# Kernel tuning notes

Hardware: AMD Instinct MI355X
Metric: run time of the kernel (lower is better)

## Reference

```python
import jax, jax.numpy as jnp
import numpy as np

V = 50257
H = 1032          # hidden_size + 8
IN = 2 * H        # gru input size
S = 8192          # encoder seq len


def setup_inputs() -> dict:
    key = jax.random.key(0)
    ks = jax.random.split(key, 12)
    s = 0.02
    return {
        "word_input": jax.random.randint(ks[0], (1,), 0, V),
        "last_context": jax.random.normal(ks[1], (1, 1, H), jnp.float32),
        "prev_hidden": jax.random.normal(ks[2], (1, 1, H), jnp.float32),
        "encoder_outputs": jax.random.normal(ks[3], (S, 1, H), jnp.float32),
        "emb": jax.random.normal(ks[4], (V, H), jnp.float32) * s,
        "W_ih": jax.random.normal(ks[5], (3 * H, IN), jnp.float32) * s,
        "W_hh": jax.random.normal(ks[6], (3 * H, H), jnp.float32) * s,
        "b_ih": jnp.zeros((3 * H,), jnp.float32),
        "b_hh": jnp.zeros((3 * H,), jnp.float32),
        "W_a": jax.random.normal(ks[7], (H, H), jnp.float32) * s,
        "b_a": jnp.zeros((H,), jnp.float32),
        "W_out": jax.random.normal(ks[8], (V, 2 * H), jnp.float32) * s,
        "b_out": jnp.zeros((V,), jnp.float32),
    }


def reference(word_input, last_context, prev_hidden, encoder_outputs,
              emb, W_ih, W_hh, b_ih, b_hh, W_a, b_a, W_out, b_out):
    # --- embedding + concat with last context -> GRU input [1, 2H]
    embedded = emb[word_input].reshape(1, H)            # dropout = identity (eval)
    x = jnp.concatenate([embedded, last_context[0]], axis=1)   # [1, 2H]
    h = prev_hidden[0]                                  # [1, H]

    # --- single-step GRU (PyTorch gate layout: r, z, n)
    gx = x @ W_ih.T + b_ih                              # [1, 3H]
    gh = h @ W_hh.T + b_hh                              # [1, 3H]
    xr, xz, xn = jnp.split(gx, 3, axis=1)
    hr, hz, hn = jnp.split(gh, 3, axis=1)
    r = jax.nn.sigmoid(xr + hr)
    z = jax.nn.sigmoid(xz + hz)
    n = jnp.tanh(xn + r * hn)
    h_new = (1.0 - z) * n + z * h                       # [1, H]

    # --- Luong attention over all encoder steps in one batched matmul
    enc = encoder_outputs[:, 0, :]                      # [S, H]
    proj = enc @ W_a.T + b_a                            # [S, H]
    scores = proj @ h_new[0]                            # [S]
    attn_weights = jax.nn.softmax(scores)               # [S]
    attn_context = (attn_weights[:, None] * enc).sum(axis=0, keepdims=True)  # [1, H]

    # --- output projection + log softmax
    joined = jnp.concatenate([h_new, attn_context], axis=1)    # [1, 2H]
    output = jax.nn.log_softmax(joined @ W_out.T + b_out, axis=1)  # [1, V]

    current_hidden = h_new[None]                        # [1, 1, H]
    attn_w = attn_weights[None, None]                   # [1, 1, S]
    return output, attn_context[None], current_hidden, attn_w
```

## Files before the change

kernel.cpp:

```cpp
#include <hip/hip_runtime.h>
#include <math.h>

#define V  50257
#define H  1032
#define INW 2064
#define S  8192

#define O_CTX  50257
#define O_HID  51289
#define O_ATTN 52321

#define NPART 2048

__device__ __forceinline__ float waveReduceSum(float v) {
#pragma unroll
  for (int off = 32; off > 0; off >>= 1) v += __shfl_down(v, off);
  return v;
}

__global__ __launch_bounds__(256) void gru_kernel(
    const int* __restrict__ word, const float* __restrict__ emb,
    const float* __restrict__ lc, const float* __restrict__ ph,
    const float* __restrict__ W_ih, const float* __restrict__ W_hh,
    const float* __restrict__ b_ih, const float* __restrict__ b_hh,
    float* __restrict__ hnew, float* __restrict__ hid_out,
    float* __restrict__ v_acc) {
  int t = threadIdx.x, wave = t >> 6, lane = t & 63;
  if (blockIdx.x == 0) {
    for (int k = t; k < H; k += 256) v_acc[k] = 0.f;
  }
  int j = blockIdx.x * 4 + wave;

  const float4* erow = (const float4*)(emb + (size_t)word[0] * H);
  const float4* lc4  = (const float4*)lc;
  const float4* ph4  = (const float4*)ph;

  const float4* wr = (const float4*)(W_ih + (size_t)j * INW);
  const float4* wz = (const float4*)(W_ih + (size_t)(H + j) * INW);
  const float4* wn = (const float4*)(W_ih + (size_t)(2 * H + j) * INW);
  float sir = 0.f, siz = 0.f, sin_ = 0.f;
  for (int i = lane; i < INW / 4; i += 64) {
    float4 xv = (i < H / 4) ? erow[i] : lc4[i - H / 4];
    float4 a = wr[i]; sir  += xv.x * a.x + xv.y * a.y + xv.z * a.z + xv.w * a.w;
    float4 b = wz[i]; siz  += xv.x * b.x + xv.y * b.y + xv.z * b.z + xv.w * b.w;
    float4 c = wn[i]; sin_ += xv.x * c.x + xv.y * c.y + xv.z * c.z + xv.w * c.w;
  }
  const float4* ur = (const float4*)(W_hh + (size_t)j * H);
  const float4* uz = (const float4*)(W_hh + (size_t)(H + j) * H);
  const float4* un = (const float4*)(W_hh + (size_t)(2 * H + j) * H);
  float shr = 0.f, shz = 0.f, shn = 0.f;
  for (int i = lane; i < H / 4; i += 64) {
    float4 hv = ph4[i];
    float4 a = ur[i]; shr += hv.x * a.x + hv.y * a.y + hv.z * a.z + hv.w * a.w;
    float4 b = uz[i]; shz += hv.x * b.x + hv.y * b.y + hv.z * b.z + hv.w * b.w;
    float4 c = un[i]; shn += hv.x * c.x + hv.y * c.y + hv.z * c.z + hv.w * c.w;
  }
  sir = waveReduceSum(sir); siz = waveReduceSum(siz); sin_ = waveReduceSum(sin_);
  shr = waveReduceSum(shr); shz = waveReduceSum(shz); shn = waveReduceSum(shn);
  if (lane == 0) {
    float gr = (sir + b_ih[j])         + (shr + b_hh[j]);
    float gz = (siz + b_ih[H + j])     + (shz + b_hh[H + j]);
    float r  = 1.f / (1.f + expf(-gr));
    float z  = 1.f / (1.f + expf(-gz));
    float n  = tanhf((sin_ + b_ih[2 * H + j]) + r * (shn + b_hh[2 * H + j]));
    float hv = (1.f - z) * n + z * ph[j];
    hnew[j] = hv;
    hid_out[j] = hv;
  }
}

__global__ __launch_bounds__(256) void va_kernel(
    const float* __restrict__ W_a, const float* __restrict__ hnew,
    float* __restrict__ v, float* __restrict__ ctx) {
  int k = blockIdx.x * 256 + threadIdx.x;
  if (k >= H) return;
  if (blockIdx.y == 0) ctx[k] = 0.f;
  int j0 = blockIdx.y * 65;
  int j1 = min(j0 + 65, H);
  float acc = 0.f;
  for (int j = j0; j < j1; ++j) acc += W_a[(size_t)j * H + k] * hnew[j];
  atomicAdd(&v[k], acc);
}

__global__ __launch_bounds__(256) void scores_kernel(
    const float* __restrict__ enc, const float* __restrict__ v,
    float* __restrict__ scores) {
  int t = threadIdx.x, wave = t >> 6, lane = t & 63;
  int s = blockIdx.x * 4 + wave;
  const float4* row = (const float4*)(enc + (size_t)s * H);
  const float4* v4  = (const float4*)v;
  float acc = 0.f;
  for (int i = lane; i < H / 4; i += 64) {
    float4 a = row[i], b = v4[i];
    acc += a.x * b.x + a.y * b.y + a.z * b.z + a.w * b.w;
  }
  acc = waveReduceSum(acc);
  if (lane == 0) scores[s] = acc;
}

__global__ __launch_bounds__(256) void ctx_kernel(
    const float* __restrict__ enc, const float* __restrict__ scores,
    float* __restrict__ ctx, float* __restrict__ attn_out) {
  __shared__ float red[256];
  __shared__ float wsh[64];
  int t = threadIdx.x;
  float m = -3.4e38f;
  for (int i = t; i < S; i += 256) m = fmaxf(m, scores[i]);
  red[t] = m; __syncthreads();
  for (int off = 128; off; off >>= 1) {
    if (t < off) red[t] = fmaxf(red[t], red[t + off]);
    __syncthreads();
  }
  m = red[0]; __syncthreads();
  float s = 0.f;
  for (int i = t; i < S; i += 256) s += expf(scores[i] - m);
  red[t] = s; __syncthreads();
  for (int off = 128; off; off >>= 1) {
    if (t < off) red[t] += red[t + off];
    __syncthreads();
  }
  float inv = 1.f / red[0];
  int s0 = blockIdx.y * 64;
  if (t < 64) wsh[t] = expf(scores[s0 + t] - m) * inv;
  __syncthreads();
  if (blockIdx.x == 0 && t < 64) attn_out[s0 + t] = wsh[t];
  int k = blockIdx.x * 256 + t;
  if (k < H) {
    float acc = 0.f;
    for (int si = 0; si < 64; ++si) acc += wsh[si] * enc[(size_t)(s0 + si) * H + k];
    atomicAdd(&ctx[k], acc);
  }
}

__global__ __launch_bounds__(256) void logits_kernel(
    const float* __restrict__ hnew, const float* __restrict__ ctx,
    const float* __restrict__ W_out, const float* __restrict__ b_out,
    float* __restrict__ out, float* __restrict__ ctx_out,
    float* __restrict__ partials) {
  __shared__ __align__(16) float joined[INW];
  __shared__ float wm[4], wsv[4];
  int t = threadIdx.x;
  for (int k = t; k < H; k += 256) {
    joined[k] = hnew[k];
    joined[H + k] = ctx[k];
  }
  if (blockIdx.x == 0) {
    for (int k = t; k < H; k += 256) ctx_out[k] = ctx[k];
  }
  __syncthreads();
  int lane = t & 63, wv = t >> 6;
  int gw = blockIdx.x * 4 + wv;
  const float4* j4 = (const float4*)joined;
  float lm = -3.4e38f, ls = 0.f;
  for (int vi = gw; vi < V; vi += NPART * 4) {
    const float4* row = (const float4*)(W_out + (size_t)vi * INW);
    float acc = 0.f;
    for (int i = lane; i < INW / 4; i += 64) {
      float4 a = row[i];
      float4 b = j4[i];
      acc += a.x * b.x + a.y * b.y + a.z * b.z + a.w * b.w;
    }
    acc = waveReduceSum(acc);
    if (lane == 0) {
      float x = acc + b_out[vi];
      out[vi] = x;
      float nm = fmaxf(lm, x);
      ls = ls * expf(lm - nm) + expf(x - nm);
      lm = nm;
    }
  }
  if (lane == 0) { wm[wv] = lm; wsv[wv] = ls; }
  __syncthreads();
  if (t == 0) {
    float m = wm[0], sb = wsv[0];
    for (int i = 1; i < 4; ++i) {
      float nm = fmaxf(m, wm[i]);
      sb = sb * expf(m - nm) + wsv[i] * expf(wm[i] - nm);
      m = nm;
    }
    partials[2 * blockIdx.x]     = m;
    partials[2 * blockIdx.x + 1] = sb;
  }
}

__global__ __launch_bounds__(256) void apply_kernel(
    float* __restrict__ out, const float* __restrict__ partials) {
  __shared__ float mm[256], ssv[256];
  int t = threadIdx.x;
  float m = -3.4e38f, s = 0.f;
  for (int i = t; i < NPART; i += 256) {
    float bm = partials[2 * i], bs = partials[2 * i + 1];
    float nm = fmaxf(m, bm);
    s = s * expf(m - nm) + bs * expf(bm - nm);
    m = nm;
  }
  mm[t] = m; ssv[t] = s; __syncthreads();
  for (int off = 128; off; off >>= 1) {
    if (t < off) {
      float m2 = mm[t + off], s2 = ssv[t + off];
      float nm = fmaxf(mm[t], m2);
      ssv[t] = ssv[t] * expf(mm[t] - nm) + s2 * expf(m2 - nm);
      mm[t] = nm;
    }
    __syncthreads();
  }
  float L = mm[0] + logf(ssv[0]);
  int i = blockIdx.x * 256 + t;
  if (i < V) out[i] -= L;
}

extern "C" void kernel_launch(void* const* d_in, const int* in_sizes, int n_in,
                              void* d_out, int out_size, void* d_ws, size_t ws_size,
                              hipStream_t stream) {
  const int*   word  = (const int*)d_in[0];
  const float* lc    = (const float*)d_in[1];
  const float* ph    = (const float*)d_in[2];
  const float* enc   = (const float*)d_in[3];
  const float* emb   = (const float*)d_in[4];
  const float* W_ih  = (const float*)d_in[5];
  const float* W_hh  = (const float*)d_in[6];
  const float* b_ih  = (const float*)d_in[7];
  const float* b_hh  = (const float*)d_in[8];
  const float* W_a   = (const float*)d_in[9];
  const float* W_out = (const float*)d_in[11];
  const float* b_out = (const float*)d_in[12];
  float* out = (float*)d_out;
  float* ws  = (float*)d_ws;

  float* hnew     = ws;
  float* v        = ws + 1032;
  float* scores   = ws + 2064;
  float* ctx      = ws + 10256;
  float* partials = ws + 11288;

  gru_kernel<<<258, 256, 0, stream>>>(word, emb, lc, ph, W_ih, W_hh, b_ih, b_hh,
                                      hnew, out + O_HID, v);
  va_kernel<<<dim3(5, 16), 256, 0, stream>>>(W_a, hnew, v, ctx);
  scores_kernel<<<2048, 256, 0, stream>>>(enc, v, scores);
  ctx_kernel<<<dim3(5, 128), 256, 0, stream>>>(enc, scores, ctx, out + O_ATTN);
  logits_kernel<<<NPART, 256, 0, stream>>>(hnew, ctx, W_out, b_out, out,
                                           out + O_CTX, partials);
  apply_kernel<<<(V + 255) / 256, 256, 0, stream>>>(out, partials);
}
```

Before: 156.5 us.

## Split GRU matvec across more waves and fuse gate nonlinearity into W_a pass

The GRU step now has one wave per half-row of each of the 3H gate rows, writing partial dot products to workspace. That replaces 258 blocks where each wave handled three gate rows serially. The gate nonlinearity is recomputed inside the W_a projection kernel, which fuses the h_new finalisation with the v = W_a^T h pass. This is meant to expose more memory parallelism for the ~38 MB of GRU weights. The cost is extra workspace traffic and redundant gate evaluation across blocks.

```diff
diff --git a/kernel.cpp b/kernel.cpp
--- a/kernel.cpp
+++ b/kernel.cpp
@@ -10,7 +10,17 @@
 #define O_HID  51289
 #define O_ATTN 52321
 
-#define NPART 2048
+#define OFF_GXP  0
+#define OFF_GHP  6192
+#define OFF_HNEW 12384
+#define OFF_V    13416
+#define OFF_CTXV 14448
+#define OFF_SC   15480
+#define OFF_PART 23672
+
+#define GRU_B   1548
+#define VA_B    80
+#define NPART   2048
 
 __device__ __forceinline__ float waveReduceSum(float v) {
 #pragma unroll
@@ -18,94 +28,105 @@
   return v;
 }
 
-__global__ __launch_bounds__(256) void gru_kernel(
+__device__ __forceinline__ float dot4(const float4 a, const float4 b) {
+  return a.x * b.x + a.y * b.y + a.z * b.z + a.w * b.w;
+}
+
+__global__ __launch_bounds__(256) void gru_mv_kernel(
     const int* __restrict__ word, const float* __restrict__ emb,
     const float* __restrict__ lc, const float* __restrict__ ph,
     const float* __restrict__ W_ih, const float* __restrict__ W_hh,
+    float* __restrict__ ws) {
+  __shared__ __align__(16) float xh[INW + H];
+  float* gxp = ws + OFF_GXP;
+  float* ghp = ws + OFF_GHP;
+  int t = threadIdx.x, wv = t >> 6, lane = t & 63, b = blockIdx.x;
+  if (b == 0) for (int i = t; i < H; i += 256) (ws + OFF_V)[i] = 0.f;
+  if (b == 1) for (int i = t; i < H; i += 256) (ws + OFF_CTXV)[i] = 0.f;
+  int w0 = word[0];
+  for (int i = t; i < INW; i += 256) xh[i] = (i < H) ? emb[(size_t)w0 * H + i] : lc[i - H];
+  for (int i = t; i < H; i += 256) xh[INW + i] = ph[i];
+  __syncthreads();
+  int g = b * 4 + wv;
+  int j = g >> 1, c = g & 1;
+  const float4* wi = (const float4*)(W_ih + (size_t)j * INW + c * (INW / 2));
+  const float4* x4 = (const float4*)(xh + c * (INW / 2));
+  float a0 = 0.f;
+  for (int i = lane; i < INW / 8; i += 64) a0 += dot4(wi[i], x4[i]);
+  const float4* wh = (const float4*)(W_hh + (size_t)j * H + c * (H / 2));
+  const float4* h4 = (const float4*)(xh + INW + c * (H / 2));
+  float a1 = 0.f;
+  for (int i = lane; i < H / 8; i += 64) a1 += dot4(wh[i], h4[i]);
+  a0 = waveReduceSum(a0); a1 = waveReduceSum(a1);
+  if (lane == 0) { gxp[c * 3096 + j] = a0; ghp[c * 3096 + j] = a1; }
+}
+
+__device__ __forceinline__ float gru_elem(
+    const float* __restrict__ gxp, const float* __restrict__ ghp,
     const float* __restrict__ b_ih, const float* __restrict__ b_hh,
-    float* __restrict__ hnew, float* __restrict__ hid_out,
-    float* __restrict__ v_acc) {
-  int t = threadIdx.x, wave = t >> 6, lane = t & 63;
-  if (blockIdx.x == 0) {
-    for (int k = t; k < H; k += 256) v_acc[k] = 0.f;
-  }
-  int j = blockIdx.x * 4 + wave;
-
-  const float4* erow = (const float4*)(emb + (size_t)word[0] * H);
-  const float4* lc4  = (const float4*)lc;
-  const float4* ph4  = (const float4*)ph;
-
-  const float4* wr = (const float4*)(W_ih + (size_t)j * INW);
-  const float4* wz = (const float4*)(W_ih + (size_t)(H + j) * INW);
-  const float4* wn = (const float4*)(W_ih + (size_t)(2 * H + j) * INW);
-  float sir = 0.f, siz = 0.f, sin_ = 0.f;
-  for (int i = lane; i < INW / 4; i += 64) {
-    float4 xv = (i < H / 4) ? erow[i] : lc4[i - H / 4];
-    float4 a = wr[i]; sir  += xv.x * a.x + xv.y * a.y + xv.z * a.z + xv.w * a.w;
-    float4 b = wz[i]; siz  += xv.x * b.x + xv.y * b.y + xv.z * b.z + xv.w * b.w;
-    float4 c = wn[i]; sin_ += xv.x * c.x + xv.y * c.y + xv.z * c.z + xv.w * c.w;
-  }
-  const float4* ur = (const float4*)(W_hh + (size_t)j * H);
-  const float4* uz = (const float4*)(W_hh + (size_t)(H + j) * H);
-  const float4* un = (const float4*)(W_hh + (size_t)(2 * H + j) * H);
-  float shr = 0.f, shz = 0.f, shn = 0.f;
-  for (int i = lane; i < H / 4; i += 64) {
-    float4 hv = ph4[i];
-    float4 a = ur[i]; shr += hv.x * a.x + hv.y * a.y + hv.z * a.z + hv.w * a.w;
-    float4 b = uz[i]; shz += hv.x * b.x + hv.y * b.y + hv.z * b.z + hv.w * b.w;
-    float4 c = un[i]; shn += hv.x * c.x + hv.y * c.y + hv.z * c.z + hv.w * c.w;
-  }
-  sir = waveReduceSum(sir); siz = waveReduceSum(siz); sin_ = waveReduceSum(sin_);
-  shr = waveReduceSum(shr); shz = waveReduceSum(shz); shn = waveReduceSum(shn);
-  if (lane == 0) {
-    float gr = (sir + b_ih[j])         + (shr + b_hh[j]);
-    float gz = (siz + b_ih[H + j])     + (shz + b_hh[H + j]);
-    float r  = 1.f / (1.f + expf(-gr));
-    float z  = 1.f / (1.f + expf(-gz));
-    float n  = tanhf((sin_ + b_ih[2 * H + j]) + r * (shn + b_hh[2 * H + j]));
-    float hv = (1.f - z) * n + z * ph[j];
-    hnew[j] = hv;
-    hid_out[j] = hv;
-  }
-}
-
-__global__ __launch_bounds__(256) void va_kernel(
-    const float* __restrict__ W_a, const float* __restrict__ hnew,
-    float* __restrict__ v, float* __restrict__ ctx) {
-  int k = blockIdx.x * 256 + threadIdx.x;
-  if (k >= H) return;
-  if (blockIdx.y == 0) ctx[k] = 0.f;
-  int j0 = blockIdx.y * 65;
-  int j1 = min(j0 + 65, H);
+    const float* __restrict__ ph, int k) {
+  float gxr = gxp[k] + gxp[3096 + k],           ghr = ghp[k] + ghp[3096 + k];
+  float gxz = gxp[H + k] + gxp[3096 + H + k],   ghz = ghp[H + k] + ghp[3096 + H + k];
+  float gxn = gxp[2 * H + k] + gxp[3096 + 2 * H + k];
+  float ghn = ghp[2 * H + k] + ghp[3096 + 2 * H + k];
+  float r = 1.f / (1.f + expf(-(gxr + ghr + b_ih[k] + b_hh[k])));
+  float z = 1.f / (1.f + expf(-(gxz + ghz + b_ih[H + k] + b_hh[H + k])));
+  float n = tanhf(gxn + b_ih[2 * H + k] + r * (ghn + b_hh[2 * H + k]));
+  return (1.f - z) * n + z * ph[k];
+}
+
+__global__ __launch_bounds__(256) void vafin_kernel(
+    const float* __restrict__ W_a, const float* __restrict__ ph,
+    const float* __restrict__ b_ih, const float* __restrict__ b_hh,
+    float* __restrict__ ws, float* __restrict__ out) {
+  __shared__ float hsh[65];
+  const float* gxp = ws + OFF_GXP;
+  const float* ghp = ws + OFF_GHP;
+  int b = blockIdx.x, t = threadIdx.x;
+  if (b < VA_B) {
+    int ct = b % 5, jc = b / 5;
+    int j0 = jc * 65;
+    int nj = min(65, H - j0);
+    if (t < nj) hsh[t] = gru_elem(gxp, ghp, b_ih, b_hh, ph, j0 + t);
+    __syncthreads();
+    int k = ct * 256 + t;
+    if (k < H) {
+      float acc = 0.f;
+      for (int j = 0; j < nj; ++j) acc += W_a[(size_t)(j0 + j) * H + k] * hsh[j];
+      atomicAdd(ws + OFF_V + k, acc);
+    }
+  } else {
+    int base = (b - VA_B) * 258;
+    for (int kk = t; kk < 258; kk += 256) {
+      int k = base + kk;
+      float hv = gru_elem(gxp, ghp, b_ih, b_hh, ph, k);
+      (ws + OFF_HNEW)[k] = hv;
+      out[O_HID + k] = hv;
+    }
+  }
+}
+
+__global__ __launch_bounds__(256) void scores_kernel(
+    const float* __restrict__ enc, float* __restrict__ ws) {
+  int t = threadIdx.x, wv = t >> 6, lane = t & 63;
+  int s = blockIdx.x * 4 + wv;
+  const float4* row = (const float4*)(enc + (size_t)s * H);
+  const float4* v4  = (const float4*)(ws + OFF_V);
   float acc = 0.f;
-  for (int j = j0; j < j1; ++j) acc += W_a[(size_t)j * H + k] * hnew[j];
-  atomicAdd(&v[k], acc);
-}
-
-__global__ __launch_bounds__(256) void scores_kernel(
-    const float* __restrict__ enc, const float* __restrict__ v,
-    float* __restrict__ scores) {
-  int t = threadIdx.x, wave = t >> 6, lane = t & 63;
-  int s = blockIdx.x * 4 + wave;
-  const float4* row = (const float4*)(enc + (size_t)s * H);
-  const float4* v4  = (const float4*)v;
-  float acc = 0.f;
-  for (int i = lane; i < H / 4; i += 64) {
-    float4 a = row[i], b = v4[i];
-    acc += a.x * b.x + a.y * b.y + a.z * b.z + a.w * b.w;
-  }
+  for (int i = lane; i < H / 4; i += 64) acc += dot4(row[i], v4[i]);
   acc = waveReduceSum(acc);
-  if (lane == 0) scores[s] = acc;
+  if (lane == 0) (ws + OFF_SC)[s] = acc;
 }
 
 __global__ __launch_bounds__(256) void ctx_kernel(
-    const float* __restrict__ enc, const float* __restrict__ scores,
-    float* __restrict__ ctx, float* __restrict__ attn_out) {
+    const float* __restrict__ enc, float* __restrict__ ws,
+    float* __restrict__ out) {
   __shared__ float red[256];
   __shared__ float wsh[64];
-  int t = threadIdx.x;
+  const float* sc = ws + OFF_SC;
+  int t = threadIdx.x, b = blockIdx.x;
   float m = -3.4e38f;
-  for (int i = t; i < S; i += 256) m = fmaxf(m, scores[i]);
+  for (int i = t; i < S; i += 256) m = fmaxf(m, sc[i]);
   red[t] = m; __syncthreads();
   for (int off = 128; off; off >>= 1) {
     if (t < off) red[t] = fmaxf(red[t], red[t + off]);
@@ -113,79 +134,74 @@
   }
   m = red[0]; __syncthreads();
   float s = 0.f;
-  for (int i = t; i < S; i += 256) s += expf(scores[i] - m);
+  for (int i = t; i < S; i += 256) s += expf(sc[i] - m);
   red[t] = s; __syncthreads();
   for (int off = 128; off; off >>= 1) {
     if (t < off) red[t] += red[t + off];
     __syncthreads();
   }
   float inv = 1.f / red[0];
-  int s0 = blockIdx.y * 64;
-  if (t < 64) wsh[t] = expf(scores[s0 + t] - m) * inv;
-  __syncthreads();
-  if (blockIdx.x == 0 && t < 64) attn_out[s0 + t] = wsh[t];
-  int k = blockIdx.x * 256 + t;
+  int ct = b % 5, yc = b / 5;
+  int s0 = yc * 64;
+  if (t < 64) wsh[t] = expf(sc[s0 + t] - m) * inv;
+  __syncthreads();
+  if (ct == 0 && t < 64) out[O_ATTN + s0 + t] = wsh[t];
+  int k = ct * 256 + t;
   if (k < H) {
     float acc = 0.f;
     for (int si = 0; si < 64; ++si) acc += wsh[si] * enc[(size_t)(s0 + si) * H + k];
-    atomicAdd(&ctx[k], acc);
+    atomicAdd(ws + OFF_CTXV + k, acc);
   }
 }
 
 __global__ __launch_bounds__(256) void logits_kernel(
-    const float* __restrict__ hnew, const float* __restrict__ ctx,
     const float* __restrict__ W_out, const float* __restrict__ b_out,
-    float* __restrict__ out, float* __restrict__ ctx_out,
-    float* __restrict__ partials) {
+    float* __restrict__ ws, float* __restrict__ out) {
   __shared__ __align__(16) float joined[INW];
-  __shared__ float wm[4], wsv[4];
-  int t = threadIdx.x;
+  __shared__ float pm[4], psv[4];
+  int t = threadIdx.x, wv = t >> 6, lane = t & 63;
   for (int k = t; k < H; k += 256) {
-    joined[k] = hnew[k];
-    joined[H + k] = ctx[k];
-  }
+    joined[k]     = (ws + OFF_HNEW)[k];
+    joined[H + k] = (ws + OFF_CTXV)[k];
+  }
+  __syncthreads();
   if (blockIdx.x == 0) {
-    for (int k = t; k < H; k += 256) ctx_out[k] = ctx[k];
-  }
-  __syncthreads();
-  int lane = t & 63, wv = t >> 6;
+    for (int k = t; k < H; k += 256) out[O_CTX + k] = joined[H + k];
+  }
+  const float4* j4 = (const float4*)joined;
   int gw = blockIdx.x * 4 + wv;
-  const float4* j4 = (const float4*)joined;
   float lm = -3.4e38f, ls = 0.f;
-  for (int vi = gw; vi < V; vi += NPART * 4) {
-    const float4* row = (const float4*)(W_out + (size_t)vi * INW);
+  for (int r = gw; r < V; r += NPART * 4) {
+    const float4* row = (const float4*)(W_out + (size_t)r * INW);
     float acc = 0.f;
-    for (int i = lane; i < INW / 4; i += 64) {
-      float4 a = row[i];
-      float4 b = j4[i];
-      acc += a.x * b.x + a.y * b.y + a.z * b.z + a.w * b.w;
-    }
+    for (int i = lane; i < INW / 4; i += 64) acc += dot4(row[i], j4[i]);
     acc = waveReduceSum(acc);
     if (lane == 0) {
-      float x = acc + b_out[vi];
-      out[vi] = x;
+      float x = acc + b_out[r];
+      out[r] = x;
       float nm = fmaxf(lm, x);
       ls = ls * expf(lm - nm) + expf(x - nm);
       lm = nm;
     }
   }
-  if (lane == 0) { wm[wv] = lm; wsv[wv] = ls; }
+  if (lane == 0) { pm[wv] = lm; psv[wv] = ls; }
   __syncthreads();
   if (t == 0) {
-    float m = wm[0], sb = wsv[0];
-    for (int i = 1; i < 4; ++i) {
-      float nm = fmaxf(m, wm[i]);
-      sb = sb * expf(m - nm) + wsv[i] * expf(wm[i] - nm);
+    float m = pm[0], sb = psv[0];
+    for (int q = 1; q < 4; ++q) {
+      float nm = fmaxf(m, pm[q]);
+      sb = sb * expf(m - nm) + psv[q] * expf(pm[q] - nm);
       m = nm;
     }
-    partials[2 * blockIdx.x]     = m;
-    partials[2 * blockIdx.x + 1] = sb;
+    (ws + OFF_PART)[2 * blockIdx.x]     = m;
+    (ws + OFF_PART)[2 * blockIdx.x + 1] = sb;
   }
 }
 
 __global__ __launch_bounds__(256) void apply_kernel(
-    float* __restrict__ out, const float* __restrict__ partials) {
+    float* __restrict__ out, const float* __restrict__ ws) {
   __shared__ float mm[256], ssv[256];
+  const float* partials = ws + OFF_PART;
   int t = threadIdx.x;
   float m = -3.4e38f, s = 0.f;
   for (int i = t; i < NPART; i += 256) {
@@ -227,18 +243,10 @@
   float* out = (float*)d_out;
   float* ws  = (float*)d_ws;
 
-  float* hnew     = ws;
-  float* v        = ws + 1032;
-  float* scores   = ws + 2064;
-  float* ctx      = ws + 10256;
-  float* partials = ws + 11288;
-
-  gru_kernel<<<258, 256, 0, stream>>>(word, emb, lc, ph, W_ih, W_hh, b_ih, b_hh,
-                                      hnew, out + O_HID, v);
-  va_kernel<<<dim3(5, 16), 256, 0, stream>>>(W_a, hnew, v, ctx);
-  scores_kernel<<<2048, 256, 0, stream>>>(enc, v, scores);
-  ctx_kernel<<<dim3(5, 128), 256, 0, stream>>>(enc, scores, ctx, out + O_ATTN);
-  logits_kernel<<<NPART, 256, 0, stream>>>(hnew, ctx, W_out, b_out, out,
-                                           out + O_CTX, partials);
-  apply_kernel<<<(V + 255) / 256, 256, 0, stream>>>(out, partials);
-}
+  gru_mv_kernel<<<GRU_B, 256, 0, stream>>>(word, emb, lc, ph, W_ih, W_hh, ws);
+  vafin_kernel<<<VA_B + 4, 256, 0, stream>>>(W_a, ph, b_ih, b_hh, ws, out);
+  scores_kernel<<<2048, 256, 0, stream>>>(enc, ws);
+  ctx_kernel<<<640, 256, 0, stream>>>(enc, ws, out);
+  logits_kernel<<<NPART, 256, 0, stream>>>(W_out, b_out, ws, out);
+  apply_kernel<<<(V + 255) / 256, 256, 0, stream>>>(out, ws);
+}
```

Measured after the change: 143.5 us. -8.3%, faster.
